# Optimization experiments

Measured on AMD Instinct MI355X. Metric: run time of the kernel, lower is better.

## Reference

```python
import jax, jax.numpy as jnp
import numpy as np

D_MODEL = 1024
N_HEADS = 16
HEAD_DIM = D_MODEL // N_HEADS


def setup_inputs() -> dict:
    key = jax.random.key(0)
    ks = jax.random.split(key, 10)
    B, NQ, S = 8, 64, 4096
    inv = 1.0 / np.sqrt(D_MODEL)
    inp = {
        "queries": jax.random.normal(ks[0], (B, NQ, D_MODEL), dtype=jnp.float32),
        "context": jax.random.normal(ks[1], (B, S, D_MODEL), dtype=jnp.float32),
        "wq": jax.random.normal(ks[2], (D_MODEL, D_MODEL), dtype=jnp.float32) * inv,
        "bq": jnp.zeros((D_MODEL,), dtype=jnp.float32),
        "wk": jax.random.normal(ks[3], (D_MODEL, D_MODEL), dtype=jnp.float32) * inv,
        "bk": jnp.zeros((D_MODEL,), dtype=jnp.float32),
        "wv": jax.random.normal(ks[4], (D_MODEL, D_MODEL), dtype=jnp.float32) * inv,
        "bv": jnp.zeros((D_MODEL,), dtype=jnp.float32),
        "wo": jax.random.normal(ks[5], (D_MODEL, D_MODEL), dtype=jnp.float32) * inv,
        "bo": jnp.zeros((D_MODEL,), dtype=jnp.float32),
    }
    return inp


def reference(queries, context, wq, bq, wk, bk, wv, bv, wo, bo):
    B, NQ, D = queries.shape
    S = context.shape[1]
    H, HD = N_HEADS, HEAD_DIM
    scale = HD ** -0.5
    # projections (x @ W^T + b, matching nn.Linear)
    q = queries @ wq.T + bq            # (B, NQ, D)
    k = context @ wk.T + bk            # (B, S, D)
    v = context @ wv.T + bv            # (B, S, D)
    q = q.reshape(B, NQ, H, HD).transpose(0, 2, 1, 3)  # (B, H, NQ, HD)
    k = k.reshape(B, S, H, HD).transpose(0, 2, 1, 3)   # (B, H, S, HD)
    v = v.reshape(B, S, H, HD).transpose(0, 2, 1, 3)   # (B, H, S, HD)
    attn = jnp.einsum('bhnd,bhsd->bhns', q, k) * scale
    attn = jax.nn.softmax(attn, axis=-1)
    # dropout is identity at eval / p=0
    out = jnp.einsum('bhns,bhsd->bhnd', attn, v)        # (B, H, NQ, HD)
    out = out.transpose(0, 2, 1, 3).reshape(B, NQ, D)   # (B, NQ, D)
    return out @ wo.T + bo
```

## Files before the change

### kernel.cpp

```cpp
#include <hip/hip_runtime.h>
#include <stdint.h>

#define BATCH   8
#define NQL     64
#define SLEN    4096
#define DMODEL  1024
#define NHEADS  16
#define HDIM    64
#define NSPLIT  8

typedef float          f32x4  __attribute__((ext_vector_type(4)));
typedef __bf16         bf16x8 __attribute__((ext_vector_type(8)));
typedef unsigned int   u32x4  __attribute__((ext_vector_type(4)));
typedef unsigned short u16x4  __attribute__((ext_vector_type(4)));
typedef unsigned short u16x8  __attribute__((ext_vector_type(8)));

__device__ __forceinline__ unsigned short f2bf(float f) {
  unsigned int u = __builtin_bit_cast(unsigned int, f);
  u += 0x7FFFu + ((u >> 16) & 1u);
  return (unsigned short)(u >> 16);
}

__device__ __forceinline__ f32x4 mfma16(bf16x8 a, bf16x8 b, f32x4 c) {
  return __builtin_amdgcn_mfma_f32_16x16x32_bf16(a, b, c, 0, 0, 0);
}

__device__ __forceinline__ bf16x8 lds_frag(const char* p) {
  u32x4 v = *(const u32x4*)p;
  return __builtin_bit_cast(bf16x8, v);
}

__device__ __forceinline__ void gload_lds16(const void* g, void* l) {
  __builtin_amdgcn_global_load_lds((const __attribute__((address_space(1))) void*)g,
                                   (__attribute__((address_space(3))) void*)l, 16, 0, 0);
}

__global__ __launch_bounds__(256)
void cvt6_kernel(const float* __restrict__ p0, const float* __restrict__ p1,
                 const float* __restrict__ p2, const float* __restrict__ p3,
                 const float* __restrict__ p4, const float* __restrict__ p5,
                 unsigned short* __restrict__ o0, unsigned short* __restrict__ o1,
                 unsigned short* __restrict__ o2, unsigned short* __restrict__ o3,
                 unsigned short* __restrict__ o4, unsigned short* __restrict__ o5) {
  int i = blockIdx.x * 256 + threadIdx.x;
  const float* src; unsigned short* dst; int rel;
  if      (i < 4194304) { src = p0; dst = o0; rel = i; }
  else if (i < 4259840) { src = p1; dst = o1; rel = i - 4194304; }
  else if (i < 4390912) { src = p2; dst = o2; rel = i - 4259840; }
  else if (i < 4521984) { src = p3; dst = o3; rel = i - 4390912; }
  else if (i < 4653056) { src = p4; dst = o4; rel = i - 4521984; }
  else                  { src = p5; dst = o5; rel = i - 4653056; }
  const float4* p = (const float4*)src + (size_t)rel * 2;
  float4 a = p[0], b = p[1];
  u16x8 o;
  o[0] = f2bf(a.x); o[1] = f2bf(a.y); o[2] = f2bf(a.z); o[3] = f2bf(a.w);
  o[4] = f2bf(b.x); o[5] = f2bf(b.y); o[6] = f2bf(b.z); o[7] = f2bf(b.w);
  *((u16x8*)dst + rel) = o;
}

template<int MODE>
__global__ __launch_bounds__(256)
void gemm_bt(const unsigned short* __restrict__ A, const unsigned short* __restrict__ Bw,
             const float* __restrict__ bias, void* __restrict__ Cout,
             int M, int N, int K) {
  __shared__ char lds[65536];

  const int tid  = threadIdx.x;
  const int wave = tid >> 6, lane = tid & 63;
  const int g    = lane >> 4, ln = lane & 15;

  const int nwg = (int)gridDim.x;
  const int cpx = nwg >> 3;
  const int bid = (int)blockIdx.x;
  const int wg  = (bid & 7) * cpx + (bid >> 3);
  const int nbn  = N >> 7;
  const int brow = (wg / nbn) << 7;
  const int bcol = (wg % nbn) << 7;
  const int wr   = wave >> 1, wc = wave & 1;

  f32x4 acc[4][4];
#pragma unroll
  for (int i = 0; i < 4; ++i)
#pragma unroll
    for (int j = 0; j < 4; ++j) acc[i][j] = (f32x4){0.f, 0.f, 0.f, 0.f};

  const int KT = K >> 6;
  const int srow = lane >> 3;
  const int srcs = (lane & 7) ^ (srow & 7);

  auto stage = [&](int kt, char* buf) {
#pragma unroll
    for (int c = wave; c < 16; c += 4) {
      int row = (c << 3) + srow;
      const char* ga = (const char*)A + (((size_t)(brow + row) * K + (kt << 6) + (srcs << 3)) << 1);
      gload_lds16(ga, buf + (c << 10));
      const char* gb = (const char*)Bw + (((size_t)(bcol + row) * K + (kt << 6) + (srcs << 3)) << 1);
      gload_lds16(gb, buf + 16384 + (c << 10));
    }
  };

  stage(0, lds);
  for (int kt = 0; kt < KT; ++kt) {
    char* cur = lds + ((kt & 1) << 15);
    if (kt + 1 < KT) {
      stage(kt + 1, lds + (((kt + 1) & 1) << 15));
      asm volatile("s_waitcnt vmcnt(8)" ::: "memory");
    } else {
      asm volatile("s_waitcnt vmcnt(0)" ::: "memory");
    }
    __builtin_amdgcn_s_barrier();
    __builtin_amdgcn_sched_barrier(0);

#pragma unroll
    for (int ks = 0; ks < 2; ++ks) {
      bf16x8 af[4], bfr[4];
      const int slot = ((ks << 2) + g) ^ (ln & 7);
#pragma unroll
      for (int mt = 0; mt < 4; ++mt) {
        int row = wr * 64 + mt * 16 + ln;
        af[mt] = lds_frag(cur + row * 128 + (slot << 4));
      }
#pragma unroll
      for (int nt = 0; nt < 4; ++nt) {
        int row = wc * 64 + nt * 16 + ln;
        bfr[nt] = lds_frag(cur + 16384 + row * 128 + (slot << 4));
      }
      __builtin_amdgcn_s_setprio(1);
#pragma unroll
      for (int mt = 0; mt < 4; ++mt)
#pragma unroll
        for (int nt = 0; nt < 4; ++nt)
          acc[mt][nt] = mfma16(af[mt], bfr[nt], acc[mt][nt]);
      __builtin_amdgcn_s_setprio(0);
    }
    __builtin_amdgcn_s_barrier();
  }

#pragma unroll
  for (int mt = 0; mt < 4; ++mt) {
#pragma unroll
    for (int nt = 0; nt < 4; ++nt) {
      f32x4 v = acc[mt][nt];
      int r0 = brow + wr * 64 + mt * 16 + g * 4;
      int c  = bcol + wc * 64 + nt * 16 + ln;
      float bi = bias[c];
      if constexpr (MODE == 0) {
        unsigned short* Cb = (unsigned short*)Cout;
#pragma unroll
        for (int j = 0; j < 4; ++j) Cb[(size_t)(r0 + j) * N + c] = f2bf(v[j] + bi);
      } else if constexpr (MODE == 1) {
        float* Cf = (float*)Cout;
#pragma unroll
        for (int j = 0; j < 4; ++j) Cf[(size_t)(r0 + j) * N + c] = v[j] + bi;
      } else {
        u16x4 pk;
#pragma unroll
        for (int j = 0; j < 4; ++j) pk[j] = f2bf(v[j] + bi);
        size_t base = ((size_t)(r0 >> 12) * 1024 + c) * 4096 + (size_t)(r0 & 4095);
        *(u16x4*)((unsigned short*)Cout + base) = pk;
      }
    }
  }
}

__global__ __launch_bounds__(256)
void attn_split(const unsigned short* __restrict__ Qp,
                const unsigned short* __restrict__ Kp,
                const unsigned short* __restrict__ Vt,
                float* __restrict__ Opart,
                float* __restrict__ Mpart,
                float* __restrict__ Lpart) {
  __shared__ char ldsKV[2][16384];
  __shared__ unsigned int plds[4 * 16 * 36];

  const int bh = (int)blockIdx.x / NSPLIT;
  const int sp = (int)blockIdx.x % NSPLIT;
  const int b = bh >> 4, h = bh & 15;
  const int tid = threadIdx.x;
  const int wave = tid >> 6, lane = tid & 63;
  const int g = lane >> 4, ln = lane & 15;
  const int pbase = wave * 576 + ln * 36;
  const int srow = lane >> 3;
  const int srcs = (lane & 7) ^ (srow & 7);

  const unsigned short* qb =
      Qp + ((size_t)(b * 64 + wave * 16 + ln) * 1024) + h * 64 + g * 8;
  bf16x8 qf[2];
  qf[0] = __builtin_bit_cast(bf16x8, *(const u32x4*)qb);
  qf[1] = __builtin_bit_cast(bf16x8, *(const u32x4*)(qb + 32));

  f32x4 oacc[4];
#pragma unroll
  for (int i = 0; i < 4; ++i) oacc[i] = (f32x4){0.f, 0.f, 0.f, 0.f};
  float mrun = -1e30f, lrun = 0.f;

  auto stage = [&](int t, int buf) {
    int s0 = t << 6;
    char* bK = ldsKV[buf];
#pragma unroll
    for (int c4 = 0; c4 < 4; ++c4) {
      int c = wave * 4 + c4;
      int cc = c & 7;
      int row = (cc << 3) + srow;
      const char* gsrc;
      if (c < 8)
        gsrc = (const char*)Kp + (((size_t)((b << 12) + s0 + row) * 1024 + (h << 6) + (srcs << 3)) << 1);
      else
        gsrc = (const char*)Vt + (((size_t)((b << 10) + (h << 6) + row) * 4096 + s0 + (srcs << 3)) << 1);
      gload_lds16(gsrc, bK + ((c < 8) ? 0 : 8192) + (cc << 10));
    }
  };

  const int T0 = sp * (SLEN / 64 / NSPLIT);
  const int NTL = SLEN / 64 / NSPLIT;
  stage(T0, 0);
  for (int tl = 0; tl < NTL; ++tl) {
    asm volatile("s_waitcnt vmcnt(0)" ::: "memory");
    __syncthreads();
    if (tl + 1 < NTL) stage(T0 + tl + 1, (tl + 1) & 1);

    char* bufK = ldsKV[tl & 1];
    char* bufV = bufK + 8192;

    f32x4 s4[4];
#pragma unroll
    for (int i = 0; i < 4; ++i) s4[i] = (f32x4){0.f, 0.f, 0.f, 0.f};
    __builtin_amdgcn_s_setprio(1);
#pragma unroll
    for (int ks = 0; ks < 2; ++ks) {
      const int slot = ((ks << 2) + g) ^ (ln & 7);
#pragma unroll
      for (int mt = 0; mt < 4; ++mt) {
        int row = mt * 16 + ln;
        s4[mt] = mfma16(lds_frag(bufK + row * 128 + (slot << 4)), qf[ks], s4[mt]);
      }
    }
    __builtin_amdgcn_s_setprio(0);

    float tmax = -1e30f;
#pragma unroll
    for (int mt = 0; mt < 4; ++mt)
#pragma unroll
      for (int j = 0; j < 4; ++j) {
        float sv = s4[mt][j] * 0.125f;
        s4[mt][j] = sv;
        tmax = fmaxf(tmax, sv);
      }
    tmax = fmaxf(tmax, __shfl_xor(tmax, 16));
    tmax = fmaxf(tmax, __shfl_xor(tmax, 32));
    float mnew = fmaxf(mrun, tmax);
    float factor = __expf(mrun - mnew);
    float psum = 0.f;
#pragma unroll
    for (int mt = 0; mt < 4; ++mt) {
      float p0 = __expf(s4[mt][0] - mnew);
      float p1 = __expf(s4[mt][1] - mnew);
      float p2 = __expf(s4[mt][2] - mnew);
      float p3 = __expf(s4[mt][3] - mnew);
      psum += (p0 + p1) + (p2 + p3);
      plds[pbase + mt * 8 + g * 2 + 0] = (unsigned)f2bf(p0) | ((unsigned)f2bf(p1) << 16);
      plds[pbase + mt * 8 + g * 2 + 1] = (unsigned)f2bf(p2) | ((unsigned)f2bf(p3) << 16);
    }
    psum += __shfl_xor(psum, 16);
    psum += __shfl_xor(psum, 32);
    lrun = lrun * factor + psum;
    mrun = mnew;

    float fj0 = __shfl(factor, g * 4 + 0);
    float fj1 = __shfl(factor, g * 4 + 1);
    float fj2 = __shfl(factor, g * 4 + 2);
    float fj3 = __shfl(factor, g * 4 + 3);
#pragma unroll
    for (int nt = 0; nt < 4; ++nt) {
      oacc[nt][0] *= fj0; oacc[nt][1] *= fj1; oacc[nt][2] *= fj2; oacc[nt][3] *= fj3;
    }

    __builtin_amdgcn_s_setprio(1);
#pragma unroll
    for (int kt2 = 0; kt2 < 2; ++kt2) {
      u32x4 pv;
      int pidx = pbase + kt2 * 16 + g * 4;
      pv[0] = plds[pidx]; pv[1] = plds[pidx + 1]; pv[2] = plds[pidx + 2]; pv[3] = plds[pidx + 3];
      bf16x8 pa = __builtin_bit_cast(bf16x8, pv);
      const int slot = ((kt2 << 2) + g) ^ (ln & 7);
#pragma unroll
      for (int nt = 0; nt < 4; ++nt) {
        int row = nt * 16 + ln;
        oacc[nt] = mfma16(pa, lds_frag(bufV + row * 128 + (slot << 4)), oacc[nt]);
      }
    }
    __builtin_amdgcn_s_setprio(0);
  }

  const int rowb = sp * (BATCH * NHEADS * 64) + bh * 64;
#pragma unroll
  for (int nt = 0; nt < 4; ++nt) {
#pragma unroll
    for (int j = 0; j < 4; ++j) {
      int q = wave * 16 + g * 4 + j;
      Opart[(size_t)(rowb + q) * 64 + nt * 16 + ln] = oacc[nt][j];
    }
  }
  if (g == 0) {
    Mpart[rowb + wave * 16 + ln] = mrun;
    Lpart[rowb + wave * 16 + ln] = lrun;
  }
}

__global__ __launch_bounds__(256)
void attn_combine(const float* __restrict__ Opart, const float* __restrict__ Mpart,
                  const float* __restrict__ Lpart, unsigned short* __restrict__ Aout) {
  const int blk = blockIdx.x;
  const int bh = blk >> 4;
  const int q  = ((blk & 15) << 2) + (threadIdx.x >> 6);
  const int hd = threadIdx.x & 63;
  const int row = bh * 64 + q;

  float mi[NSPLIT];
  float M = -1e30f;
#pragma unroll
  for (int i = 0; i < NSPLIT; ++i) {
    mi[i] = Mpart[i * 8192 + row];
    M = fmaxf(M, mi[i]);
  }
  float L = 0.f, o = 0.f;
#pragma unroll
  for (int i = 0; i < NSPLIT; ++i) {
    float w = __expf(mi[i] - M);
    L += Lpart[i * 8192 + row] * w;
    o += Opart[(size_t)(i * 8192 + row) * 64 + hd] * w;
  }
  const int b = bh >> 4, h = bh & 15;
  Aout[(size_t)(b * 64 + q) * 1024 + h * 64 + hd] = f2bf(o / L);
}

extern "C" void kernel_launch(void* const* d_in, const int* in_sizes, int n_in,
                              void* d_out, int out_size, void* d_ws, size_t ws_size,
                              hipStream_t stream) {
  const float* queries = (const float*)d_in[0];
  const float* context = (const float*)d_in[1];
  const float* wq = (const float*)d_in[2];
  const float* bq = (const float*)d_in[3];
  const float* wk = (const float*)d_in[4];
  const float* bk = (const float*)d_in[5];
  const float* wv = (const float*)d_in[6];
  const float* bv = (const float*)d_in[7];
  const float* wo = (const float*)d_in[8];
  const float* bo = (const float*)d_in[9];

  const size_t CTX_E = (size_t)BATCH * SLEN * DMODEL;
  const size_t QRY_E = (size_t)BATCH * NQL * DMODEL;
  const size_t W_E   = (size_t)DMODEL * DMODEL;

  char* ws = (char*)d_ws;
  size_t off = 0;
  auto alloc = [&](size_t bytes) {
    char* p = ws + off;
    off += (bytes + 255) & ~(size_t)255;
    return p;
  };
  unsigned short* ctx_bf = (unsigned short*)alloc(CTX_E * 2);
  unsigned short* q_bf   = (unsigned short*)alloc(QRY_E * 2);
  unsigned short* wq_bf  = (unsigned short*)alloc(W_E * 2);
  unsigned short* wk_bf  = (unsigned short*)alloc(W_E * 2);
  unsigned short* wv_bf  = (unsigned short*)alloc(W_E * 2);
  unsigned short* wo_bf  = (unsigned short*)alloc(W_E * 2);
  unsigned short* Qp     = (unsigned short*)alloc(QRY_E * 2);
  unsigned short* Kp     = (unsigned short*)alloc(CTX_E * 2);
  unsigned short* Vt     = (unsigned short*)alloc(CTX_E * 2);
  unsigned short* Ao     = (unsigned short*)alloc(QRY_E * 2);
  if (off > ws_size) return;

  float* Opart = (float*)ctx_bf;
  float* Mpart = Opart + (size_t)NSPLIT * BATCH * NHEADS * 64 * 64;
  float* Lpart = Mpart + (size_t)NSPLIT * BATCH * NHEADS * 64;

  cvt6_kernel<<<dim3(18688), 256, 0, stream>>>(context, queries, wq, wk, wv, wo,
                                               ctx_bf, q_bf, wq_bf, wk_bf, wv_bf, wo_bf);

  const int M_KV = BATCH * SLEN;
  const int M_Q  = BATCH * NQL;

  gemm_bt<0><<<dim3((M_KV / 128) * (DMODEL / 128)), 256, 0, stream>>>(ctx_bf, wk_bf, bk, Kp, M_KV, DMODEL, DMODEL);
  gemm_bt<2><<<dim3((M_KV / 128) * (DMODEL / 128)), 256, 0, stream>>>(ctx_bf, wv_bf, bv, Vt, M_KV, DMODEL, DMODEL);

  gemm_bt<0><<<dim3((M_Q / 128) * (DMODEL / 128)), 256, 0, stream>>>(q_bf, wq_bf, bq, Qp, M_Q, DMODEL, DMODEL);

  attn_split<<<dim3(BATCH * NHEADS * NSPLIT), 256, 0, stream>>>(Qp, Kp, Vt, Opart, Mpart, Lpart);
  attn_combine<<<dim3(BATCH * NHEADS * 16), 256, 0, stream>>>(Opart, Mpart, Lpart, Ao);

  gemm_bt<1><<<dim3((M_Q / 128) * (DMODEL / 128)), 256, 0, stream>>>(Ao, wo_bf, bo, d_out, M_Q, DMODEL, DMODEL);
}
```

Measured before the change: 435.7 us.

## Fuse projection GEMMs, fold attention combine into split kernel, single-buffer GEMM

Merges the K, V and Q projection GEMMs into one launch that dispatches on block index. The split-attention combine step moves into the last finishing split block per head, using an atomic counter that the conversion kernel zeroes. The conversion kernel becomes a grid-stride loop over fewer blocks. The GEMM body drops LDS double buffering and the explicit vmcnt pipelining in favour of a single 32KB buffer with __syncthreads, which may expose load latency but halves LDS use and so could raise occupancy.

```diff
diff --git a/kernel.cpp b/kernel.cpp
--- a/kernel.cpp
+++ b/kernel.cpp
@@ -35,47 +35,49 @@
                                    (__attribute__((address_space(3))) void*)l, 16, 0, 0);
 }
 
+#define CVT_TOT   4784128
+#define CVT_STEP  (2048 * 256)
 __global__ __launch_bounds__(256)
 void cvt6_kernel(const float* __restrict__ p0, const float* __restrict__ p1,
                  const float* __restrict__ p2, const float* __restrict__ p3,
                  const float* __restrict__ p4, const float* __restrict__ p5,
                  unsigned short* __restrict__ o0, unsigned short* __restrict__ o1,
                  unsigned short* __restrict__ o2, unsigned short* __restrict__ o3,
-                 unsigned short* __restrict__ o4, unsigned short* __restrict__ o5) {
-  int i = blockIdx.x * 256 + threadIdx.x;
-  const float* src; unsigned short* dst; int rel;
-  if      (i < 4194304) { src = p0; dst = o0; rel = i; }
-  else if (i < 4259840) { src = p1; dst = o1; rel = i - 4194304; }
-  else if (i < 4390912) { src = p2; dst = o2; rel = i - 4259840; }
-  else if (i < 4521984) { src = p3; dst = o3; rel = i - 4390912; }
-  else if (i < 4653056) { src = p4; dst = o4; rel = i - 4521984; }
-  else                  { src = p5; dst = o5; rel = i - 4653056; }
-  const float4* p = (const float4*)src + (size_t)rel * 2;
-  float4 a = p[0], b = p[1];
-  u16x8 o;
-  o[0] = f2bf(a.x); o[1] = f2bf(a.y); o[2] = f2bf(a.z); o[3] = f2bf(a.w);
-  o[4] = f2bf(b.x); o[5] = f2bf(b.y); o[6] = f2bf(b.z); o[7] = f2bf(b.w);
-  *((u16x8*)dst + rel) = o;
+                 unsigned short* __restrict__ o4, unsigned short* __restrict__ o5,
+                 unsigned int* __restrict__ cnt) {
+  if (blockIdx.x == 0 && threadIdx.x < BATCH * NHEADS) cnt[threadIdx.x] = 0u;
+  for (int i = blockIdx.x * 256 + threadIdx.x; i < CVT_TOT; i += CVT_STEP) {
+    const float* src; unsigned short* dst; int rel;
+    if      (i < 4194304) { src = p0; dst = o0; rel = i; }
+    else if (i < 4259840) { src = p1; dst = o1; rel = i - 4194304; }
+    else if (i < 4390912) { src = p2; dst = o2; rel = i - 4259840; }
+    else if (i < 4521984) { src = p3; dst = o3; rel = i - 4390912; }
+    else if (i < 4653056) { src = p4; dst = o4; rel = i - 4521984; }
+    else                  { src = p5; dst = o5; rel = i - 4653056; }
+    const float4* p = (const float4*)src + (size_t)rel * 2;
+    float4 a = p[0], b = p[1];
+    u16x8 o;
+    o[0] = f2bf(a.x); o[1] = f2bf(a.y); o[2] = f2bf(a.z); o[3] = f2bf(a.w);
+    o[4] = f2bf(b.x); o[5] = f2bf(b.y); o[6] = f2bf(b.z); o[7] = f2bf(b.w);
+    *((u16x8*)dst + rel) = o;
+  }
 }
 
 template<int MODE>
-__global__ __launch_bounds__(256)
-void gemm_bt(const unsigned short* __restrict__ A, const unsigned short* __restrict__ Bw,
-             const float* __restrict__ bias, void* __restrict__ Cout,
-             int M, int N, int K) {
-  __shared__ char lds[65536];
-
+__device__ __forceinline__
+void gemm_body(char* lds, const unsigned short* __restrict__ A,
+               const unsigned short* __restrict__ Bw, const float* __restrict__ bias,
+               void* __restrict__ Cout, int M, int lb) {
+  const int K = 1024, N = 1024;
   const int tid  = threadIdx.x;
   const int wave = tid >> 6, lane = tid & 63;
   const int g    = lane >> 4, ln = lane & 15;
 
-  const int nwg = (int)gridDim.x;
+  const int nwg = (M >> 7) << 3;
   const int cpx = nwg >> 3;
-  const int bid = (int)blockIdx.x;
-  const int wg  = (bid & 7) * cpx + (bid >> 3);
-  const int nbn  = N >> 7;
-  const int brow = (wg / nbn) << 7;
-  const int bcol = (wg % nbn) << 7;
+  const int wg  = (lb & 7) * cpx + (lb >> 3);
+  const int brow = (wg >> 3) << 7;
+  const int bcol = (wg & 7) << 7;
   const int wr   = wave >> 1, wc = wave & 1;
 
   f32x4 acc[4][4];
@@ -84,32 +86,17 @@
 #pragma unroll
     for (int j = 0; j < 4; ++j) acc[i][j] = (f32x4){0.f, 0.f, 0.f, 0.f};
 
-  const int KT = K >> 6;
   const int srow = lane >> 3;
   const int srcs = (lane & 7) ^ (srow & 7);
 
-  auto stage = [&](int kt, char* buf) {
+  for (int kt = 0; kt < 16; ++kt) {
 #pragma unroll
     for (int c = wave; c < 16; c += 4) {
       int row = (c << 3) + srow;
-      const char* ga = (const char*)A + (((size_t)(brow + row) * K + (kt << 6) + (srcs << 3)) << 1);
-      gload_lds16(ga, buf + (c << 10));
-      const char* gb = (const char*)Bw + (((size_t)(bcol + row) * K + (kt << 6) + (srcs << 3)) << 1);
-      gload_lds16(gb, buf + 16384 + (c << 10));
-    }
-  };
-
-  stage(0, lds);
-  for (int kt = 0; kt < KT; ++kt) {
-    char* cur = lds + ((kt & 1) << 15);
-    if (kt + 1 < KT) {
-      stage(kt + 1, lds + (((kt + 1) & 1) << 15));
-      asm volatile("s_waitcnt vmcnt(8)" ::: "memory");
-    } else {
-      asm volatile("s_waitcnt vmcnt(0)" ::: "memory");
-    }
-    __builtin_amdgcn_s_barrier();
-    __builtin_amdgcn_sched_barrier(0);
+      gload_lds16(A + (size_t)(brow + row) * K + (kt << 6) + (srcs << 3), lds + (c << 10));
+      gload_lds16(Bw + (size_t)(bcol + row) * K + (kt << 6) + (srcs << 3), lds + 16384 + (c << 10));
+    }
+    __syncthreads();
 
 #pragma unroll
     for (int ks = 0; ks < 2; ++ks) {
@@ -118,12 +105,12 @@
 #pragma unroll
       for (int mt = 0; mt < 4; ++mt) {
         int row = wr * 64 + mt * 16 + ln;
-        af[mt] = lds_frag(cur + row * 128 + (slot << 4));
+        af[mt] = lds_frag(lds + row * 128 + (slot << 4));
       }
 #pragma unroll
       for (int nt = 0; nt < 4; ++nt) {
         int row = wc * 64 + nt * 16 + ln;
-        bfr[nt] = lds_frag(cur + 16384 + row * 128 + (slot << 4));
+        bfr[nt] = lds_frag(lds + 16384 + row * 128 + (slot << 4));
       }
       __builtin_amdgcn_s_setprio(1);
 #pragma unroll
@@ -133,7 +120,7 @@
           acc[mt][nt] = mfma16(af[mt], bfr[nt], acc[mt][nt]);
       __builtin_amdgcn_s_setprio(0);
     }
-    __builtin_amdgcn_s_barrier();
+    __syncthreads();
   }
 
 #pragma unroll
@@ -164,14 +151,39 @@
 }
 
 __global__ __launch_bounds__(256)
+void proj3_kernel(const unsigned short* __restrict__ ctx_bf, const unsigned short* __restrict__ q_bf,
+                  const unsigned short* __restrict__ wk_bf, const unsigned short* __restrict__ wv_bf,
+                  const unsigned short* __restrict__ wq_bf,
+                  const float* __restrict__ bk, const float* __restrict__ bv,
+                  const float* __restrict__ bq,
+                  unsigned short* __restrict__ Kp, unsigned short* __restrict__ Vt,
+                  unsigned short* __restrict__ Qp) {
+  __shared__ char lds[32768];
+  const int bid = (int)blockIdx.x;
+  if (bid < 2048)       gemm_body<0>(lds, ctx_bf, wk_bf, bk, Kp, BATCH * SLEN, bid);
+  else if (bid < 4096)  gemm_body<2>(lds, ctx_bf, wv_bf, bv, Vt, BATCH * SLEN, bid - 2048);
+  else                  gemm_body<0>(lds, q_bf, wq_bf, bq, Qp, BATCH * NQL, bid - 4096);
+}
+
+__global__ __launch_bounds__(256)
+void gemm_o_kernel(const unsigned short* __restrict__ Ao, const unsigned short* __restrict__ wo_bf,
+                   const float* __restrict__ bo, float* __restrict__ out) {
+  __shared__ char lds[32768];
+  gemm_body<1>(lds, Ao, wo_bf, bo, out, BATCH * NQL, (int)blockIdx.x);
+}
+
+__global__ __launch_bounds__(256)
 void attn_split(const unsigned short* __restrict__ Qp,
                 const unsigned short* __restrict__ Kp,
                 const unsigned short* __restrict__ Vt,
                 float* __restrict__ Opart,
                 float* __restrict__ Mpart,
-                float* __restrict__ Lpart) {
+                float* __restrict__ Lpart,
+                unsigned int* __restrict__ cnt,
+                unsigned short* __restrict__ Aout) {
   __shared__ char ldsKV[2][16384];
   __shared__ unsigned int plds[4 * 16 * 36];
+  __shared__ unsigned int lastflag;
 
   const int bh = (int)blockIdx.x / NSPLIT;
   const int sp = (int)blockIdx.x % NSPLIT;
@@ -305,33 +317,38 @@
     Mpart[rowb + wave * 16 + ln] = mrun;
     Lpart[rowb + wave * 16 + ln] = lrun;
   }
-}
-
-__global__ __launch_bounds__(256)
-void attn_combine(const float* __restrict__ Opart, const float* __restrict__ Mpart,
-                  const float* __restrict__ Lpart, unsigned short* __restrict__ Aout) {
-  const int blk = blockIdx.x;
-  const int bh = blk >> 4;
-  const int q  = ((blk & 15) << 2) + (threadIdx.x >> 6);
-  const int hd = threadIdx.x & 63;
-  const int row = bh * 64 + q;
-
-  float mi[NSPLIT];
-  float M = -1e30f;
-#pragma unroll
-  for (int i = 0; i < NSPLIT; ++i) {
-    mi[i] = Mpart[i * 8192 + row];
-    M = fmaxf(M, mi[i]);
-  }
-  float L = 0.f, o = 0.f;
-#pragma unroll
-  for (int i = 0; i < NSPLIT; ++i) {
-    float w = __expf(mi[i] - M);
-    L += Lpart[i * 8192 + row] * w;
-    o += Opart[(size_t)(i * 8192 + row) * 64 + hd] * w;
-  }
-  const int b = bh >> 4, h = bh & 15;
-  Aout[(size_t)(b * 64 + q) * 1024 + h * 64 + hd] = f2bf(o / L);
+
+  __threadfence();
+  __syncthreads();
+  if (tid == 0) {
+    unsigned int prev = __hip_atomic_fetch_add(&cnt[bh], 1u, __ATOMIC_ACQ_REL,
+                                               __HIP_MEMORY_SCOPE_AGENT);
+    lastflag = (prev == NSPLIT - 1) ? 1u : 0u;
+  }
+  __syncthreads();
+  if (lastflag) {
+    const int hd = tid & 63;
+    const int q0 = (tid >> 6) << 4;
+    for (int qq = 0; qq < 16; ++qq) {
+      const int q = q0 + qq;
+      const int row = bh * 64 + q;
+      float mi[NSPLIT];
+      float Mx = -1e30f;
+#pragma unroll
+      for (int i = 0; i < NSPLIT; ++i) {
+        mi[i] = Mpart[i * 8192 + row];
+        Mx = fmaxf(Mx, mi[i]);
+      }
+      float L = 0.f, o = 0.f;
+#pragma unroll
+      for (int i = 0; i < NSPLIT; ++i) {
+        float w = __expf(mi[i] - Mx);
+        L += Lpart[i * 8192 + row] * w;
+        o += Opart[(size_t)(i * 8192 + row) * 64 + hd] * w;
+      }
+      Aout[(size_t)(b * 64 + q) * 1024 + h * 64 + hd] = f2bf(o / L);
+    }
+  }
 }
 
 extern "C" void kernel_launch(void* const* d_in, const int* in_sizes, int n_in,
@@ -369,25 +386,21 @@
   unsigned short* Kp     = (unsigned short*)alloc(CTX_E * 2);
   unsigned short* Vt     = (unsigned short*)alloc(CTX_E * 2);
   unsigned short* Ao     = (unsigned short*)alloc(QRY_E * 2);
+  unsigned int*   cnt    = (unsigned int*)alloc(BATCH * NHEADS * sizeof(unsigned int));
   if (off > ws_size) return;
 
   float* Opart = (float*)ctx_bf;
   float* Mpart = Opart + (size_t)NSPLIT * BATCH * NHEADS * 64 * 64;
   float* Lpart = Mpart + (size_t)NSPLIT * BATCH * NHEADS * 64;
 
-  cvt6_kernel<<<dim3(18688), 256, 0, stream>>>(context, queries, wq, wk, wv, wo,
-                                               ctx_bf, q_bf, wq_bf, wk_bf, wv_bf, wo_bf);
-
-  const int M_KV = BATCH * SLEN;
-  const int M_Q  = BATCH * NQL;
-
-  gemm_bt<0><<<dim3((M_KV / 128) * (DMODEL / 128)), 256, 0, stream>>>(ctx_bf, wk_bf, bk, Kp, M_KV, DMODEL, DMODEL);
-  gemm_bt<2><<<dim3((M_KV / 128) * (DMODEL / 128)), 256, 0, stream>>>(ctx_bf, wv_bf, bv, Vt, M_KV, DMODEL, DMODEL);
-
-  gemm_bt<0><<<dim3((M_Q / 128) * (DMODEL / 128)), 256, 0, stream>>>(q_bf, wq_bf, bq, Qp, M_Q, DMODEL, DMODEL);
-
-  attn_split<<<dim3(BATCH * NHEADS * NSPLIT), 256, 0, stream>>>(Qp, Kp, Vt, Opart, Mpart, Lpart);
-  attn_combine<<<dim3(BATCH * NHEADS * 16), 256, 0, stream>>>(Opart, Mpart, Lpart, Ao);
-
-  gemm_bt<1><<<dim3((M_Q / 128) * (DMODEL / 128)), 256, 0, stream>>>(Ao, wo_bf, bo, d_out, M_Q, DMODEL, DMODEL);
-}
+  cvt6_kernel<<<dim3(2048), 256, 0, stream>>>(context, queries, wq, wk, wv, wo,
+                                              ctx_bf, q_bf, wq_bf, wk_bf, wv_bf, wo_bf, cnt);
+
+  proj3_kernel<<<dim3(4128), 256, 0, stream>>>(ctx_bf, q_bf, wk_bf, wv_bf, wq_bf,
+                                               bk, bv, bq, Kp, Vt, Qp);
+
+  attn_split<<<dim3(BATCH * NHEADS * NSPLIT), 256, 0, stream>>>(Qp, Kp, Vt, Opart, Mpart,
+                                                                Lpart, cnt, Ao);
+
+  gemm_o_kernel<<<dim3(32), 256, 0, stream>>>(Ao, wo_bf, bo, (float*)d_out);
+}
```

Result: slower. 578.9 us (+32.9%).
